# Kernel tuning notes

Hardware: AMD Instinct MI355X
Metric: run time of the kernel (lower is better)

Reference implementation:

```python
import jax, jax.numpy as jnp
import numpy as np

F, OUT = 256, 16
H = [128, 128, 64]
B = 8192


def _normed(v, g):
    # weight_norm (torch default dim=0): w[o,:] = g[o] * v[o,:] / ||v[o,:]||
    # v: [F, out, in], g: [F, out]
    return g[..., None] * v / jnp.linalg.norm(v, axis=-1, keepdims=True)


def setup_inputs() -> dict:
    key = jax.random.key(0)
    ks = jax.random.split(key, 12)
    s = 0.1
    return {
        "tabular": jax.random.normal(ks[0], (B, 2, F), dtype=jnp.float32),
        # input layer: Linear(1, H[0]) per feature, stacked over F
        "v_in": jax.random.normal(ks[1], (F, H[0], 1), dtype=jnp.float32) * s,
        "g_in": jnp.ones((F, H[0]), dtype=jnp.float32),
        "b_in": jax.random.normal(ks[2], (F, H[0]), dtype=jnp.float32) * s,
        # dense_0: Linear(H[0], H[1])
        "v_h0": jax.random.normal(ks[3], (F, H[1], H[0]), dtype=jnp.float32) * s,
        "g_h0": jnp.ones((F, H[1]), dtype=jnp.float32),
        "b_h0": jax.random.normal(ks[4], (F, H[1]), dtype=jnp.float32) * s,
        # dense_1: Linear(H[1], H[2])
        "v_h1": jax.random.normal(ks[5], (F, H[2], H[1]), dtype=jnp.float32) * s,
        "g_h1": jnp.ones((F, H[2]), dtype=jnp.float32),
        "b_h1": jax.random.normal(ks[6], (F, H[2]), dtype=jnp.float32) * s,
        # dense_out: Linear(H[2], OUT, bias=False)
        "v_out": jax.random.normal(ks[7], (F, OUT, H[2]), dtype=jnp.float32) * s,
        "g_out": jnp.ones((F, OUT), dtype=jnp.float32),
        "bias": jnp.zeros((1, OUT), dtype=jnp.float32),
    }


def reference(tabular, v_in, g_in, b_in, v_h0, g_h0, b_h0, v_h1, g_h1, b_h1,
              v_out, g_out, bias):
    values, is_missing = tabular[:, 0, :], tabular[:, 1, :]  # [B, F]
    x = values * (1.0 - is_missing)
    # input layer: in-dim is 1, so it's an outer product with the weight column
    w0 = _normed(v_in, g_in)[:, :, 0]                       # [F, H0]
    h = jax.nn.relu(x[:, :, None] * w0[None] + b_in[None])  # [B, F, H0]
    # hidden layers (dropout is identity in eval mode)
    h = jax.nn.relu(jnp.einsum("bfi,foi->bfo", h, _normed(v_h0, g_h0)) + b_h0[None])
    h = jax.nn.relu(jnp.einsum("bfi,foi->bfo", h, _normed(v_h1, g_h1)) + b_h1[None])
    outputs = jnp.einsum("bfi,foi->bfo", h, _normed(v_out, g_out))  # [B, F, OUT]
    # feature_dropout is identity in eval mode
    logits = jnp.sum(outputs, axis=1) + bias                # [B, OUT]
    return logits, outputs
```

## Files before the change

kernel.cpp:

```cpp
#include <hip/hip_runtime.h>

typedef unsigned short u16;
typedef unsigned int   u32;
typedef __attribute__((ext_vector_type(8))) short bf16x8;
typedef __attribute__((ext_vector_type(4))) float f32x4;
typedef __attribute__((ext_vector_type(2))) float f32x2;

#define NFEAT  256
#define NBATCH 8192
#define BT     64
#define NBT    (NBATCH / BT)
#define ITERS  8

__device__ __forceinline__ u16 f2bf(float f) {
    u32 u = __builtin_bit_cast(u32, f);
    return (u16)((u + 0x7FFFu + ((u >> 16) & 1u)) >> 16);
}
__device__ __forceinline__ u32 cvtpk(float a, float b) {
    u32 r;
    asm("v_cvt_pk_bf16_f32 %0, %1, %2" : "=v"(r) : "v"(a), "v"(b));
    return r;
}
__device__ __forceinline__ f32x4 mfma16(bf16x8 a, bf16x8 b, f32x4 c) {
    return __builtin_amdgcn_mfma_f32_16x16x32_bf16(a, b, c, 0, 0, 0);
}
__device__ __forceinline__ bf16x8 frag_word0(u32 word0) {
    union { bf16x8 v; u32 w[4]; } u;
    u.w[0] = word0; u.w[1] = 0; u.w[2] = 0; u.w[3] = 0;
    return u.v;
}
__device__ __forceinline__ char* swz(char* base, int b, int col2) {
    return base + b * 256 + (col2 ^ ((b & 15) << 4));
}
__device__ __forceinline__ const char* swz(const char* base, int b, int col2) {
    return base + b * 256 + (col2 ^ ((b & 15) << 4));
}

__global__ void prep_w0(const float* __restrict__ v_in, const float* __restrict__ g_in,
                        u16* __restrict__ w0) {
    int i = blockIdx.x * blockDim.x + threadIdx.x;
    float v = v_in[i];
    float g = g_in[i];
    w0[i] = f2bf(v >= 0.f ? g : -g);
}

__global__ void prep_norm(const float* __restrict__ v_h0, const float* __restrict__ g_h0,
                          const float* __restrict__ v_h1, const float* __restrict__ g_h1,
                          const float* __restrict__ v_out, const float* __restrict__ g_out,
                          u16* __restrict__ w1, u16* __restrict__ w2, u16* __restrict__ w3) {
    const int wave = (blockIdx.x * blockDim.x + threadIdx.x) >> 6;
    const int lane = threadIdx.x & 63;
    if (wave < 32768 + 16384) {
        const float* src; u16* dst; float g;
        if (wave < 32768) {
            src = v_h0 + (size_t)wave * 128; dst = w1 + (size_t)wave * 128; g = g_h0[wave];
        } else {
            int r = wave - 32768;
            src = v_h1 + (size_t)r * 128; dst = w2 + (size_t)r * 128; g = g_h1[r];
        }
        f32x2 v = *(const f32x2*)(src + lane * 2);
        float ss = v.x * v.x + v.y * v.y;
        #pragma unroll
        for (int off = 32; off; off >>= 1) ss += __shfl_xor(ss, off);
        float s = g * rsqrtf(ss);
        *(u32*)(dst + lane * 2) = cvtpk(v.x * s, v.y * s);
    } else {
        int r = wave - 49152;
        const float* src = v_out + (size_t)r * 64;
        float v = src[lane];
        float ss = v * v;
        #pragma unroll
        for (int off = 32; off; off >>= 1) ss += __shfl_xor(ss, off);
        float s = g_out[r] * rsqrtf(ss);
        w3[(size_t)r * 64 + lane] = f2bf(v * s);
    }
}

__global__ void prep_x(const float* __restrict__ tab, u16* __restrict__ x_t) {
    __shared__ u16 tile[64][65];
    const int bb = (blockIdx.x % (NBATCH / 64)) * 64;
    const int ff = (blockIdx.x / (NBATCH / 64)) * 64;
    const int tr = threadIdx.x >> 6;
    const int tc = threadIdx.x & 63;
    #pragma unroll
    for (int i = 0; i < 16; i++) {
        int b = bb + tr + i * 4;
        float val  = tab[(size_t)b * 512 + ff + tc];
        float miss = tab[(size_t)b * 512 + 256 + ff + tc];
        tile[tr + i * 4][tc] = f2bf(val * (1.f - miss));
    }
    __syncthreads();
    #pragma unroll
    for (int i = 0; i < 16; i++) {
        int fr = tr + i * 4;
        x_t[(size_t)(ff + fr) * NBATCH + bb + tc] = tile[tc][fr];
    }
}

__global__ void reduce_logits(const float* __restrict__ outputs,
                              const float* __restrict__ bias,
                              float* __restrict__ logits) {
    const int b = blockIdx.x * 4 + (threadIdx.x >> 6);
    const int lane = threadIdx.x & 63;
    const int j4 = lane & 3;
    const int fo = lane >> 2;
    const float* base = outputs + (size_t)b * (NFEAT * 16);
    f32x4 acc = {};
    #pragma unroll
    for (int it = 0; it < 16; it++) {
        f32x4 v = *(const f32x4*)(base + (fo + it * 16) * 16 + j4 * 4);
        acc[0] += v[0]; acc[1] += v[1]; acc[2] += v[2]; acc[3] += v[3];
    }
    #pragma unroll
    for (int off = 4; off < 64; off <<= 1) {
        acc[0] += __shfl_xor(acc[0], off);
        acc[1] += __shfl_xor(acc[1], off);
        acc[2] += __shfl_xor(acc[2], off);
        acc[3] += __shfl_xor(acc[3], off);
    }
    if (lane < 4) {
        f32x4 bs = *(const f32x4*)(bias + lane * 4);
        acc[0] += bs[0]; acc[1] += bs[1]; acc[2] += bs[2]; acc[3] += bs[3];
        *(f32x4*)(logits + b * 16 + lane * 4) = acc;
    }
}

__global__ __launch_bounds__(128, 2) void nam_main(
    const u16* __restrict__ x_t, const u16* __restrict__ w0g,
    const u16* __restrict__ w1g, const u16* __restrict__ w2g, const u16* __restrict__ w3g,
    const float* __restrict__ b_in, const float* __restrict__ b_h0, const float* __restrict__ b_h1,
    float* __restrict__ outputs)
{
    __shared__ u16 hA[BT * 128];
    __shared__ u16 hB[BT * 128];

    const int bid   = blockIdx.x;
    const int f     = (bid & 7) * 32 + ((bid >> 3) & 31);
    const int chunk = bid >> 8;
    const int t  = threadIdx.x;
    const int w  = t >> 6;
    const int lane = t & 63;
    const int lo = lane & 15;
    const int hi = lane >> 4;

    u32 w0w[4];  float biw[4];
    #pragma unroll
    for (int m = 0; m < 4; m++) {
        const int o = f * 128 + w * 64 + m * 16 + lo;
        w0w[m] = (u32)w0g[o];
        biw[m] = b_in[o];
    }
    bf16x8 w1f[4][4];
    {
        const u16* base = w1g + ((size_t)(f * 128 + w * 64 + lo)) * 128 + hi * 8;
        #pragma unroll
        for (int m = 0; m < 4; m++)
            #pragma unroll
            for (int ks = 0; ks < 4; ks++)
                w1f[m][ks] = *(const bf16x8*)(base + m * 16 * 128 + ks * 32);
    }
    bf16x8 w2f[2][4];
    {
        const u16* base = w2g + ((size_t)(f * 64 + w * 32 + lo)) * 128 + hi * 8;
        #pragma unroll
        for (int m = 0; m < 2; m++)
            #pragma unroll
            for (int ks = 0; ks < 4; ks++)
                w2f[m][ks] = *(const bf16x8*)(base + m * 16 * 128 + ks * 32);
    }
    bf16x8 w3f[2];
    {
        const u16* base = w3g + ((size_t)(f * 16 + lo)) * 64 + hi * 8;
        #pragma unroll
        for (int ks = 0; ks < 2; ks++)
            w3f[ks] = *(const bf16x8*)(base + ks * 32);
    }
    f32x4 bs1[4];
    #pragma unroll
    for (int m = 0; m < 4; m++)
        bs1[m] = *(const f32x4*)(b_h0 + f * 128 + w * 64 + m * 16 + hi * 4);
    f32x4 bs2[2];
    #pragma unroll
    for (int m = 0; m < 2; m++)
        bs2[m] = *(const f32x4*)(b_h1 + f * 64 + w * 32 + m * 16 + hi * 4);
    bf16x8 a0[4];
    #pragma unroll
    for (int m = 0; m < 4; m++) {
        u32 pk = w0w[m] | (cvtpk(biw[m], biw[m]) << 16);
        a0[m] = frag_word0(hi == 0 ? pk : 0u);
    }

    for (int it = 0; it < ITERS; it++) {
        const int bt = chunk * ITERS + it;
        u32 xw[4];
        #pragma unroll
        for (int n = 0; n < 4; n++)
            xw[n] = (u32)x_t[(size_t)f * NBATCH + bt * BT + n * 16 + lo];

        __syncthreads();

        {
            bf16x8 bm[4];
            #pragma unroll
            for (int n = 0; n < 4; n++) {
                u32 pk = xw[n] | 0x3F800000u;
                bm[n] = frag_word0(hi == 0 ? pk : 0u);
            }
            #pragma unroll
            for (int m = 0; m < 4; m++) {
                #pragma unroll
                for (int n = 0; n < 4; n++) {
                    f32x4 d = mfma16(a0[m], bm[n], f32x4{});
                    const int b = n * 16 + lo;
                    const int col2 = (w * 64 + m * 16 + hi * 4) * 2;
                    *(uint2*)swz((char*)hA, b, col2) =
                        make_uint2(cvtpk(fmaxf(0.f, d[0]), fmaxf(0.f, d[1])),
                                   cvtpk(fmaxf(0.f, d[2]), fmaxf(0.f, d[3])));
                }
            }
        }
        __syncthreads();

        {
            f32x4 acc[4][4] = {};
            #pragma unroll
            for (int ks = 0; ks < 4; ks++) {
                bf16x8 bm[4];
                #pragma unroll
                for (int n = 0; n < 4; n++) {
                    const int b = n * 16 + lo;
                    bm[n] = *(const bf16x8*)swz((const char*)hA, b, ks * 64 + hi * 16);
                }
                __builtin_amdgcn_s_setprio(1);
                #pragma unroll
                for (int m = 0; m < 4; m++)
                    #pragma unroll
                    for (int n = 0; n < 4; n++)
                        acc[m][n] = mfma16(w1f[m][ks], bm[n], acc[m][n]);
                __builtin_amdgcn_s_setprio(0);
            }
            #pragma unroll
            for (int m = 0; m < 4; m++) {
                const int col2 = (w * 64 + m * 16 + hi * 4) * 2;
                #pragma unroll
                for (int n = 0; n < 4; n++) {
                    const int b = n * 16 + lo;
                    float r0 = fmaxf(0.f, acc[m][n][0] + bs1[m][0]);
                    float r1 = fmaxf(0.f, acc[m][n][1] + bs1[m][1]);
                    float r2 = fmaxf(0.f, acc[m][n][2] + bs1[m][2]);
                    float r3 = fmaxf(0.f, acc[m][n][3] + bs1[m][3]);
                    *(uint2*)swz((char*)hB, b, col2) =
                        make_uint2(cvtpk(r0, r1), cvtpk(r2, r3));
                }
            }
        }
        __syncthreads();

        {
            f32x4 acc[2][4] = {};
            #pragma unroll
            for (int ks = 0; ks < 4; ks++) {
                bf16x8 bm[4];
                #pragma unroll
                for (int n = 0; n < 4; n++) {
                    const int b = n * 16 + lo;
                    bm[n] = *(const bf16x8*)swz((const char*)hB, b, ks * 64 + hi * 16);
                }
                __builtin_amdgcn_s_setprio(1);
                #pragma unroll
                for (int m = 0; m < 2; m++)
                    #pragma unroll
                    for (int n = 0; n < 4; n++)
                        acc[m][n] = mfma16(w2f[m][ks], bm[n], acc[m][n]);
                __builtin_amdgcn_s_setprio(0);
            }
            #pragma unroll
            for (int m = 0; m < 2; m++) {
                const int col2 = (w * 32 + m * 16 + hi * 4) * 2;
                #pragma unroll
                for (int n = 0; n < 4; n++) {
                    const int b = n * 16 + lo;
                    float r0 = fmaxf(0.f, acc[m][n][0] + bs2[m][0]);
                    float r1 = fmaxf(0.f, acc[m][n][1] + bs2[m][1]);
                    float r2 = fmaxf(0.f, acc[m][n][2] + bs2[m][2]);
                    float r3 = fmaxf(0.f, acc[m][n][3] + bs2[m][3]);
                    *(uint2*)swz((char*)hA, b, col2) =
                        make_uint2(cvtpk(r0, r1), cvtpk(r2, r3));
                }
            }
        }
        __syncthreads();

        {
            f32x4 acc[2] = {};
            #pragma unroll
            for (int ks = 0; ks < 2; ks++) {
                #pragma unroll
                for (int n = 0; n < 2; n++) {
                    const int b = w * 32 + n * 16 + lo;
                    bf16x8 bm = *(const bf16x8*)swz((const char*)hA, b, ks * 64 + hi * 16);
                    acc[n] = mfma16(w3f[ks], bm, acc[n]);
                }
            }
            #pragma unroll
            for (int n = 0; n < 2; n++) {
                const int gb = bt * BT + w * 32 + n * 16 + lo;
                float* op = outputs + ((size_t)gb * NFEAT + f) * 16 + hi * 4;
                *(f32x4*)op = acc[n];
            }
        }
    }
}

extern "C" void kernel_launch(void* const* d_in, const int* in_sizes, int n_in,
                              void* d_out, int out_size, void* d_ws, size_t ws_size,
                              hipStream_t stream) {
    const float* tab   = (const float*)d_in[0];
    const float* v_in  = (const float*)d_in[1];
    const float* g_in  = (const float*)d_in[2];
    const float* b_in  = (const float*)d_in[3];
    const float* v_h0  = (const float*)d_in[4];
    const float* g_h0  = (const float*)d_in[5];
    const float* b_h0  = (const float*)d_in[6];
    const float* v_h1  = (const float*)d_in[7];
    const float* g_h1  = (const float*)d_in[8];
    const float* b_h1  = (const float*)d_in[9];
    const float* v_out = (const float*)d_in[10];
    const float* g_out = (const float*)d_in[11];
    const float* bias  = (const float*)d_in[12];

    char* ws = (char*)d_ws;
    u16* w0  = (u16*)(ws);
    u16* w1  = (u16*)(ws + 65536);
    u16* w2  = (u16*)(ws + 65536 + 8388608);
    u16* w3  = (u16*)(ws + 12648448);
    u16* x_t = (u16*)(ws + 13172736);

    float* logits  = (float*)d_out;
    float* outputs = (float*)d_out + (size_t)NBATCH * 16;

    hipLaunchKernelGGL(prep_w0,   dim3(128),   dim3(256), 0, stream, v_in, g_in, w0);
    hipLaunchKernelGGL(prep_norm, dim3(13312), dim3(256), 0, stream,
                       v_h0, g_h0, v_h1, g_h1, v_out, g_out, w1, w2, w3);
    hipLaunchKernelGGL(prep_x,    dim3(512),   dim3(256), 0, stream, tab, x_t);
    hipLaunchKernelGGL(nam_main,  dim3(NFEAT * NBT / ITERS), dim3(128), 0, stream,
                       x_t, w0, w1, w2, w3, b_in, b_h0, b_h1, outputs);
    hipLaunchKernelGGL(reduce_logits, dim3(NBATCH / 4), dim3(256), 0, stream,
                       outputs, bias, logits);
}
```

Before: 180.6 us.

## Stream layer weights from global per iteration to raise occupancy to three blocks

Instead of holding all dense_0, dense_out weights and biases in registers for the whole block, the kernel now reloads dense_0 weight fragments from global (L2-cached) each iteration with a one-step software prefetch across k-slices. dense_out weights and the biases are also reloaded per iteration. Launch bounds go from 2 to 3 blocks per CU. The aim is lower register pressure and more resident waves to hide latency, at the cost of repeated weight loads per tile.

```diff
diff --git a/kernel.cpp b/kernel.cpp
--- a/kernel.cpp
+++ b/kernel.cpp
@@ -34,6 +34,9 @@
 }
 __device__ __forceinline__ const char* swz(const char* base, int b, int col2) {
     return base + b * 256 + (col2 ^ ((b & 15) << 4));
+}
+__device__ __forceinline__ u32 relu_pk(float v0, float v1, float b0, float b1) {
+    return cvtpk(fmaxf(v0 + b0, 0.f), fmaxf(v1 + b1, 0.f));
 }
 
 __global__ void prep_w0(const float* __restrict__ v_in, const float* __restrict__ g_in,
@@ -59,11 +62,11 @@
             src = v_h1 + (size_t)r * 128; dst = w2 + (size_t)r * 128; g = g_h1[r];
         }
         f32x2 v = *(const f32x2*)(src + lane * 2);
-        float ss = v.x * v.x + v.y * v.y;
+        float ss = v[0] * v[0] + v[1] * v[1];
         #pragma unroll
         for (int off = 32; off; off >>= 1) ss += __shfl_xor(ss, off);
         float s = g * rsqrtf(ss);
-        *(u32*)(dst + lane * 2) = cvtpk(v.x * s, v.y * s);
+        *(u32*)(dst + lane * 2) = cvtpk(v[0] * s, v[1] * s);
     } else {
         int r = wave - 49152;
         const float* src = v_out + (size_t)r * 64;
@@ -125,7 +128,7 @@
     }
 }
 
-__global__ __launch_bounds__(128, 2) void nam_main(
+__global__ __launch_bounds__(128, 3) void nam_main(
     const u16* __restrict__ x_t, const u16* __restrict__ w0g,
     const u16* __restrict__ w1g, const u16* __restrict__ w2g, const u16* __restrict__ w3g,
     const float* __restrict__ b_in, const float* __restrict__ b_h0, const float* __restrict__ b_h1,
@@ -143,21 +146,12 @@
     const int lo = lane & 15;
     const int hi = lane >> 4;
 
-    u32 w0w[4];  float biw[4];
+    u32 a0pk[4];
     #pragma unroll
     for (int m = 0; m < 4; m++) {
         const int o = f * 128 + w * 64 + m * 16 + lo;
-        w0w[m] = (u32)w0g[o];
-        biw[m] = b_in[o];
-    }
-    bf16x8 w1f[4][4];
-    {
-        const u16* base = w1g + ((size_t)(f * 128 + w * 64 + lo)) * 128 + hi * 8;
-        #pragma unroll
-        for (int m = 0; m < 4; m++)
-            #pragma unroll
-            for (int ks = 0; ks < 4; ks++)
-                w1f[m][ks] = *(const bf16x8*)(base + m * 16 * 128 + ks * 32);
+        float bi = b_in[o];
+        a0pk[m] = (u32)w0g[o] | (cvtpk(bi, bi) << 16);
     }
     bf16x8 w2f[2][4];
     {
@@ -168,49 +162,34 @@
             for (int ks = 0; ks < 4; ks++)
                 w2f[m][ks] = *(const bf16x8*)(base + m * 16 * 128 + ks * 32);
     }
-    bf16x8 w3f[2];
-    {
-        const u16* base = w3g + ((size_t)(f * 16 + lo)) * 64 + hi * 8;
-        #pragma unroll
-        for (int ks = 0; ks < 2; ks++)
-            w3f[ks] = *(const bf16x8*)(base + ks * 32);
-    }
-    f32x4 bs1[4];
-    #pragma unroll
-    for (int m = 0; m < 4; m++)
-        bs1[m] = *(const f32x4*)(b_h0 + f * 128 + w * 64 + m * 16 + hi * 4);
-    f32x4 bs2[2];
-    #pragma unroll
-    for (int m = 0; m < 2; m++)
-        bs2[m] = *(const f32x4*)(b_h1 + f * 64 + w * 32 + m * 16 + hi * 4);
-    bf16x8 a0[4];
-    #pragma unroll
-    for (int m = 0; m < 4; m++) {
-        u32 pk = w0w[m] | (cvtpk(biw[m], biw[m]) << 16);
-        a0[m] = frag_word0(hi == 0 ? pk : 0u);
-    }
+    const u16* w1base = w1g + ((size_t)(f * 128 + w * 64 + lo)) * 128 + hi * 8;
+    const u16* w3base = w3g + ((size_t)(f * 16 + lo)) * 64 + hi * 8;
 
     for (int it = 0; it < ITERS; it++) {
         const int bt = chunk * ITERS + it;
+
         u32 xw[4];
         #pragma unroll
         for (int n = 0; n < 4; n++)
             xw[n] = (u32)x_t[(size_t)f * NBATCH + bt * BT + n * 16 + lo];
+        bf16x8 wc[4];
+        #pragma unroll
+        for (int m = 0; m < 4; m++)
+            wc[m] = *(const bf16x8*)(w1base + m * 2048);
 
         __syncthreads();
 
         {
             bf16x8 bm[4];
             #pragma unroll
-            for (int n = 0; n < 4; n++) {
-                u32 pk = xw[n] | 0x3F800000u;
-                bm[n] = frag_word0(hi == 0 ? pk : 0u);
-            }
+            for (int n = 0; n < 4; n++)
+                bm[n] = frag_word0(hi == 0 ? (xw[n] | 0x3F800000u) : 0u);
             #pragma unroll
             for (int m = 0; m < 4; m++) {
-                #pragma unroll
-                for (int n = 0; n < 4; n++) {
-                    f32x4 d = mfma16(a0[m], bm[n], f32x4{});
+                bf16x8 a0 = frag_word0(hi == 0 ? a0pk[m] : 0u);
+                #pragma unroll
+                for (int n = 0; n < 4; n++) {
+                    f32x4 d = mfma16(a0, bm[n], f32x4{});
                     const int b = n * 16 + lo;
                     const int col2 = (w * 64 + m * 16 + hi * 4) * 2;
                     *(uint2*)swz((char*)hA, b, col2) =
@@ -225,6 +204,12 @@
             f32x4 acc[4][4] = {};
             #pragma unroll
             for (int ks = 0; ks < 4; ks++) {
+                bf16x8 wn[4];
+                if (ks < 3) {
+                    #pragma unroll
+                    for (int m = 0; m < 4; m++)
+                        wn[m] = *(const bf16x8*)(w1base + m * 2048 + (ks + 1) * 32);
+                }
                 bf16x8 bm[4];
                 #pragma unroll
                 for (int n = 0; n < 4; n++) {
@@ -236,27 +221,32 @@
                 for (int m = 0; m < 4; m++)
                     #pragma unroll
                     for (int n = 0; n < 4; n++)
-                        acc[m][n] = mfma16(w1f[m][ks], bm[n], acc[m][n]);
+                        acc[m][n] = mfma16(wc[m], bm[n], acc[m][n]);
                 __builtin_amdgcn_s_setprio(0);
+                if (ks < 3) {
+                    #pragma unroll
+                    for (int m = 0; m < 4; m++) wc[m] = wn[m];
+                }
             }
             #pragma unroll
             for (int m = 0; m < 4; m++) {
+                f32x4 bs = *(const f32x4*)(b_h0 + f * 128 + w * 64 + m * 16 + hi * 4);
                 const int col2 = (w * 64 + m * 16 + hi * 4) * 2;
                 #pragma unroll
                 for (int n = 0; n < 4; n++) {
                     const int b = n * 16 + lo;
-                    float r0 = fmaxf(0.f, acc[m][n][0] + bs1[m][0]);
-                    float r1 = fmaxf(0.f, acc[m][n][1] + bs1[m][1]);
-                    float r2 = fmaxf(0.f, acc[m][n][2] + bs1[m][2]);
-                    float r3 = fmaxf(0.f, acc[m][n][3] + bs1[m][3]);
-                    *(uint2*)swz((char*)hB, b, col2) =
-                        make_uint2(cvtpk(r0, r1), cvtpk(r2, r3));
+                    u32 p0 = relu_pk(acc[m][n][0], acc[m][n][1], bs[0], bs[1]);
+                    u32 p1 = relu_pk(acc[m][n][2], acc[m][n][3], bs[2], bs[3]);
+                    *(uint2*)swz((char*)hB, b, col2) = make_uint2(p0, p1);
                 }
             }
         }
         __syncthreads();
 
+        bf16x8 w3a, w3b;
         {
+            w3a = *(const bf16x8*)(w3base);
+            w3b = *(const bf16x8*)(w3base + 32);
             f32x4 acc[2][4] = {};
             #pragma unroll
             for (int ks = 0; ks < 4; ks++) {
@@ -276,16 +266,14 @@
             }
             #pragma unroll
             for (int m = 0; m < 2; m++) {
+                f32x4 bs = *(const f32x4*)(b_h1 + f * 64 + w * 32 + m * 16 + hi * 4);
                 const int col2 = (w * 32 + m * 16 + hi * 4) * 2;
                 #pragma unroll
                 for (int n = 0; n < 4; n++) {
                     const int b = n * 16 + lo;
-                    float r0 = fmaxf(0.f, acc[m][n][0] + bs2[m][0]);
-                    float r1 = fmaxf(0.f, acc[m][n][1] + bs2[m][1]);
-                    float r2 = fmaxf(0.f, acc[m][n][2] + bs2[m][2]);
-                    float r3 = fmaxf(0.f, acc[m][n][3] + bs2[m][3]);
-                    *(uint2*)swz((char*)hA, b, col2) =
-                        make_uint2(cvtpk(r0, r1), cvtpk(r2, r3));
+                    u32 p0 = relu_pk(acc[m][n][0], acc[m][n][1], bs[0], bs[1]);
+                    u32 p1 = relu_pk(acc[m][n][2], acc[m][n][3], bs[2], bs[3]);
+                    *(uint2*)swz((char*)hA, b, col2) = make_uint2(p0, p1);
                 }
             }
         }
@@ -295,11 +283,12 @@
             f32x4 acc[2] = {};
             #pragma unroll
             for (int ks = 0; ks < 2; ks++) {
+                bf16x8 a = (ks == 0) ? w3a : w3b;
                 #pragma unroll
                 for (int n = 0; n < 2; n++) {
                     const int b = w * 32 + n * 16 + lo;
                     bf16x8 bm = *(const bf16x8*)swz((const char*)hA, b, ks * 64 + hi * 16);
-                    acc[n] = mfma16(w3f[ks], bm, acc[n]);
+                    acc[n] = mfma16(a, bm, acc[n]);
                 }
             }
             #pragma unroll
```

Result: slower. 466.8 us (+158.4%).
